# Kernel tuning notes

Hardware: AMD Instinct MI355X
Metric: run time of the kernel (lower is better)

The kernel has to match this reference:

```python
import jax, jax.numpy as jnp
import numpy as np

THETA = 10000.0
EPS = 1e-6

def _rope_tables(n, d):
    # 2D image RoPE: square grid side x side, half of head-dim rotates with
    # row position, half with column position. rotate-half pairing (i, i+d/2).
    side = int(np.sqrt(n))
    dq = d // 4  # angle count per spatial axis
    inv_freq = 1.0 / (THETA ** (np.arange(dq, dtype=np.float32) / dq))
    ang = np.arange(side, dtype=np.float32)[:, None] * inv_freq[None, :]  # [side, dq]
    row = np.broadcast_to(ang[:, None, :], (side, side, dq)).reshape(n, dq)
    col = np.broadcast_to(ang[None, :, :], (side, side, dq)).reshape(n, dq)
    angles = np.concatenate([row, col], axis=-1)  # [n, d//2]
    return jnp.asarray(np.cos(angles)), jnp.asarray(np.sin(angles))

def _apply_rope(t, cos, sin):
    # t: [b, h, n, d]; cos/sin: [n, d//2]
    d2 = t.shape[-1] // 2
    t1, t2 = t[..., :d2], t[..., d2:]
    return jnp.concatenate([t1 * cos - t2 * sin, t1 * sin + t2 * cos], axis=-1)

def _rmsnorm(t, scale):
    var = jnp.mean(t * t, axis=-1, keepdims=True)
    return t * jax.lax.rsqrt(var + EPS) * scale

def setup_inputs() -> dict:
    key = jax.random.key(0)
    ks = jax.random.split(key, 3)
    B, N, D = 8, 1024, 1024
    x = jax.random.normal(ks[0], (B, N, D), dtype=jnp.float32)
    Wqkv = jax.random.normal(ks[1], (D, 3 * D), dtype=jnp.float32) * (D ** -0.5)
    bqkv = jnp.zeros((3 * D,), dtype=jnp.float32)
    Wout = jax.random.normal(ks[2], (D, D), dtype=jnp.float32) * (D ** -0.5)
    bout = jnp.zeros((D,), dtype=jnp.float32)
    hd = D // 16
    return {"x": x, "Wqkv": Wqkv, "bqkv": bqkv, "Wout": Wout, "bout": bout,
            "q_scale": jnp.ones((hd,), jnp.float32), "k_scale": jnp.ones((hd,), jnp.float32)}

def reference(x, Wqkv, bqkv, Wout, bout, q_scale, k_scale):
    B, N, D = x.shape
    H = 16
    hd = D // H
    qkv = x @ Wqkv + bqkv  # [B, N, 3D]
    qkv = qkv.reshape(B, N, 3, H, hd).transpose(2, 0, 3, 1, 4)  # [3, B, H, N, hd]
    q, k, v = qkv[0], qkv[1], qkv[2]
    q = _rmsnorm(q, q_scale)
    k = _rmsnorm(k, k_scale)
    cos, sin = _rope_tables(N, hd)
    q = _apply_rope(q, cos, sin)
    k = _apply_rope(k, cos, sin)
    scale = hd ** -0.5
    scores = jnp.einsum('bhqd,bhkd->bhqk', q, k) * scale
    attn = jax.nn.softmax(scores, axis=-1)
    o = jnp.einsum('bhqk,bhkd->bhqd', attn, v)  # [B, H, N, hd]
    o = o.transpose(0, 2, 1, 3).reshape(B, N, D)
    return o @ Wout + bout
```

## Files before the change

kernel.cpp:

```cpp
#include <hip/hip_runtime.h>
#include <hip/hip_bf16.h>
#include <hip/hip_fp16.h>
#include <math.h>

#define QSZ 8388608

typedef short bf16x8 __attribute__((ext_vector_type(8)));
typedef _Float16 f16x8 __attribute__((ext_vector_type(8)));
typedef float f32x4 __attribute__((ext_vector_type(4)));

__device__ __forceinline__ unsigned short f2bf(float f) {
  __hip_bfloat16 h = __float2bfloat16(f);
  return *reinterpret_cast<unsigned short*>(&h);
}

__device__ __forceinline__ void gload16(const void* g, void* l) {
  __builtin_amdgcn_global_load_lds(
      (const __attribute__((address_space(1))) void*)g,
      (__attribute__((address_space(3))) void*)l, 16, 0, 0);
}

__global__ __launch_bounds__(256)
void cvt_all(const float* __restrict__ x, unsigned short* __restrict__ xb,
             const float* __restrict__ Wq, unsigned short* __restrict__ wqT,
             const float* __restrict__ Wo, unsigned short* __restrict__ woT) {
  __shared__ unsigned short tile[32][33];
  const int bid = blockIdx.x;
  const int t = threadIdx.x;
  if (bid < 4096) {
    const int i = (bid * 256 + t) * 8;
    const float4 a = *(const float4*)&x[i];
    const float4 b = *(const float4*)&x[i + 4];
    ushort4 lo, hi;
    lo.x = f2bf(a.x); lo.y = f2bf(a.y); lo.z = f2bf(a.z); lo.w = f2bf(a.w);
    hi.x = f2bf(b.x); hi.y = f2bf(b.y); hi.z = f2bf(b.z); hi.w = f2bf(b.w);
    *(ushort4*)&xb[i] = lo;
    *(ushort4*)&xb[i + 4] = hi;
    return;
  }
  const float* src;
  unsigned short* dst;
  int bx, by, N;
  if (bid < 7168) {
    src = Wq; dst = wqT; N = 3072;
    bx = (bid - 4096) % 96; by = (bid - 4096) / 96;
  } else {
    src = Wo; dst = woT; N = 1024;
    bx = (bid - 7168) % 32; by = (bid - 7168) / 32;
  }
  const int k0 = by * 32, n0 = bx * 32;
  const int r = t >> 3, c4 = (t & 7) * 4;
  const float4 v = *(const float4*)&src[(k0 + r) * N + n0 + c4];
  tile[r][c4 + 0] = f2bf(v.x);
  tile[r][c4 + 1] = f2bf(v.y);
  tile[r][c4 + 2] = f2bf(v.z);
  tile[r][c4 + 3] = f2bf(v.w);
  __syncthreads();
  ushort4 o;
  o.x = tile[c4 + 0][r];
  o.y = tile[c4 + 1][r];
  o.z = tile[c4 + 2][r];
  o.w = tile[c4 + 3][r];
  *(ushort4*)&dst[(long)(n0 + r) * 1024 + k0 + c4] = o;
}

template<int MODE>
__global__ __launch_bounds__(512, 2)
void gemm256(const unsigned short* __restrict__ A,
             const unsigned short* __restrict__ Bt,
             const float* __restrict__ bias,
             float* __restrict__ Cf,
             __half* __restrict__ Ch,
             const float* __restrict__ qsc,
             const float* __restrict__ ksc) {
  __shared__ __align__(16) unsigned short As[2][16384];
  __shared__ __align__(16) unsigned short Bs[2][16384];
  __shared__ float2 Tab[512];

  constexpr int GXN = (MODE == 0) ? 12 : 4;
  constexpr int CPX = (MODE == 0) ? 48 : 16;

  const int t = threadIdx.x;
  const int swz = (blockIdx.x & 7) * CPX + (blockIdx.x >> 3);
  const int bm = swz / GXN, bn = swz % GXN;
  const int w = t >> 6, lane = t & 63;
  const int M0 = (w >> 2) * 128, N0 = (w & 3) * 64;
  const int lm = lane & 15, q4 = lane >> 4;

  if (MODE == 0) {
    const int pos = t >> 4, idx = t & 15;
    const float invf = expf(-(float)idx * 0.57564627324851149f);
    const float ang = (float)pos * invf;
    Tab[t] = make_float2(cosf(ang), sinf(ang));
  }

  const int c8 = ((t & 7) ^ ((t >> 3) & 7)) << 3;
  const unsigned short* aSrc = A + (long)(bm * 256 + (t >> 3)) * 1024 + c8;
  const unsigned short* bSrc = Bt + (long)(bn * 256 + (t >> 3)) * 1024 + c8;
  unsigned short* lA[2] = {&As[0][t * 8], &As[1][t * 8]};
  unsigned short* lB[2] = {&Bs[0][t * 8], &Bs[1][t * 8]};

  f32x4 acc[8][4] = {};

  auto stage = [&](int buf, int kt) {
    const unsigned short* a = aSrc + kt * 64;
    const unsigned short* b = bSrc + kt * 64;
    unsigned short* la = lA[buf];
    unsigned short* lb = lB[buf];
#pragma unroll
    for (int j = 0; j < 4; ++j) {
      gload16(a + j * 65536, la + j * 4096);
      gload16(b + j * 65536, lb + j * 4096);
    }
  };

  auto compute = [&](const unsigned short* Ac, const unsigned short* Bc) {
#pragma unroll
    for (int kk = 0; kk < 2; ++kk) {
      bf16x8 af[8], bg[4];
#pragma unroll
      for (int mi = 0; mi < 8; ++mi) {
        const int row = M0 + mi * 16 + lm;
        af[mi] = *(const bf16x8*)
            &Ac[row * 64 + ((((kk << 2) + q4) ^ (row & 7)) << 3)];
      }
#pragma unroll
      for (int ni = 0; ni < 4; ++ni) {
        const int row = N0 + ni * 16 + lm;
        bg[ni] = *(const bf16x8*)
            &Bc[row * 64 + ((((kk << 2) + q4) ^ (row & 7)) << 3)];
      }
#pragma unroll
      for (int mi = 0; mi < 8; ++mi)
#pragma unroll
        for (int ni = 0; ni < 4; ++ni)
          acc[mi][ni] = __builtin_amdgcn_mfma_f32_16x16x32_bf16(
              af[mi], bg[ni], acc[mi][ni], 0, 0, 0);
    }
  };

  stage(0, 0);
  stage(1, 1);
  asm volatile("s_waitcnt vmcnt(8)" ::: "memory");
  __builtin_amdgcn_s_barrier();

  for (int kt = 0; kt < 14; ++kt) {
    const int s = kt & 1;
    compute(s ? &As[1][0] : &As[0][0], s ? &Bs[1][0] : &Bs[0][0]);
    asm volatile("s_waitcnt lgkmcnt(0)" ::: "memory");
    __builtin_amdgcn_s_barrier();
    stage(s, kt + 2);
    asm volatile("s_waitcnt vmcnt(8)" ::: "memory");
    __builtin_amdgcn_s_barrier();
  }
  compute(&As[0][0], &Bs[0][0]);
  asm volatile("s_waitcnt lgkmcnt(0)" ::: "memory");
  __builtin_amdgcn_s_barrier();
  asm volatile("s_waitcnt vmcnt(0)" ::: "memory");
  __builtin_amdgcn_s_barrier();
  compute(&As[1][0], &Bs[1][0]);

  const int r0 = q4 << 2;
  const int nb = bn * 256 + N0;

  if (MODE == 1) {
#pragma unroll
    for (int mi = 0; mi < 8; ++mi)
#pragma unroll
      for (int ni = 0; ni < 4; ++ni) {
        const int n = nb + ni * 16 + lm;
        const float bvv = bias[n];
#pragma unroll
        for (int r = 0; r < 4; ++r)
          Cf[(long)(bm * 256 + M0 + mi * 16 + r0 + r) * 1024 + n] =
              acc[mi][ni][r] + bvv;
      }
    return;
  }

  const int tq = nb >> 10, h = (nb >> 6) & 15;

  if (tq == 2) {
#pragma unroll
    for (int mi = 0; mi < 8; ++mi)
#pragma unroll
      for (int ni = 0; ni < 4; ++ni) {
        const int col = nb + ni * 16 + lm;
        const int dd = col & 63;
        const float bv = bias[col];
#pragma unroll
        for (int r = 0; r < 4; ++r) {
          const int m = bm * 256 + M0 + mi * 16 + r0 + r;
          const int b = m >> 10, nn = m & 1023;
          Ch[2L * QSZ + ((long)((b * 16 + h) * 64 + dd)) * 1024 + nn] =
              __float2half(acc[mi][ni][r] + bv);
        }
      }
    return;
  }

  const float* scp = (tq == 0) ? qsc : ksc;
  const float qmul = (tq == 0) ? 0.18033688011112042f : 1.0f;
  float scv[4], bv[4];
#pragma unroll
  for (int ni = 0; ni < 4; ++ni) {
    scv[ni] = scp[ni * 16 + lm];
    bv[ni] = bias[nb + ni * 16 + lm];
  }
  __half* base = Ch + (long)tq * QSZ;
#pragma unroll
  for (int mi = 0; mi < 8; ++mi) {
#pragma unroll
    for (int r = 0; r < 4; ++r) {
      const float v0 = acc[mi][0][r] + bv[0];
      const float v1 = acc[mi][1][r] + bv[1];
      const float v2 = acc[mi][2][r] + bv[2];
      const float v3 = acc[mi][3][r] + bv[3];
      float ss = v0 * v0 + v1 * v1 + v2 * v2 + v3 * v3;
      ss += __shfl_xor(ss, 1, 64);
      ss += __shfl_xor(ss, 2, 64);
      ss += __shfl_xor(ss, 4, 64);
      ss += __shfl_xor(ss, 8, 64);
      const float inv = rsqrtf(ss * (1.0f / 64.0f) + 1e-6f) * qmul;
      const float a0 = v0 * inv * scv[0];
      const float a1 = v1 * inv * scv[1];
      const float a2 = v2 * inv * scv[2];
      const float a3 = v3 * inv * scv[3];
      const int m = bm * 256 + M0 + mi * 16 + r0 + r;
      const int b = m >> 10, nn = m & 1023;
      const float2 tr = Tab[(nn >> 5) * 16 + lm];
      const float2 tc = Tab[(nn & 31) * 16 + lm];
      __half* row = base + ((long)((b * 16 + h) * 1024 + nn)) * 64 + lm;
      row[0]  = __float2half(a0 * tr.x - a2 * tr.y);
      row[16] = __float2half(a1 * tc.x - a3 * tc.y);
      row[32] = __float2half(a0 * tr.y + a2 * tr.x);
      row[48] = __float2half(a1 * tc.y + a3 * tc.x);
    }
  }
}

__global__ __launch_bounds__(256, 3)
void attn_mfma(const __half* __restrict__ qh, const __half* __restrict__ kh,
               const __half* __restrict__ vh, unsigned short* __restrict__ ob) {
  __shared__ __align__(16) __half Ks[2][4096];
  __shared__ __align__(16) __half Vs[2][4096];
  __shared__ __align__(16) __half Pl[8][1152];
  const int t = threadIdx.x;
  const int w = t >> 6, lane = t & 63;
  const int flat = blockIdx.x + blockIdx.y * 8;
  const int xcd = flat & 7, j = flat >> 3;
  const int bh = xcd * 16 + (j >> 3);
  const int qt = j & 7;
  const int lm = lane & 15, q4 = lane >> 4;

  f16x8 qf[2][2];
#pragma unroll
  for (int g = 0; g < 2; ++g) {
    const __half* qrow =
        qh + ((long)(bh * 1024 + qt * 128 + g * 64 + w * 16 + lm)) * 64 +
        q4 * 8;
    qf[g][0] = *(const f16x8*)qrow;
    qf[g][1] = *(const f16x8*)(qrow + 32);
  }

  f32x4 o[2][4] = {};
  float l_r[2][4] = {};

  const int prow = t >> 3, pc = t & 7;
  const int scz = pc ^ (prow & 7);
  const __half* ksrc0 = kh + (long)(bh * 1024 + prow) * 64 + scz * 8;
  const __half* vsrc0 = vh + (long)(bh * 64 + prow) * 1024 + scz * 8;

  gload16(ksrc0, &Ks[0][t * 8]);
  gload16(ksrc0 + 32 * 64, &Ks[0][2048 + t * 8]);
  gload16(vsrc0, &Vs[0][t * 8]);
  gload16(vsrc0 + 32 * 1024, &Vs[0][2048 + t * 8]);

  for (int kc = 0; kc < 16; ++kc) {
    const int cur = kc & 1;
    __syncthreads();

    if (kc < 15) {
      const int nx = cur ^ 1;
      const __half* ksrc = ksrc0 + (kc + 1) * 4096;
      const __half* vsrc = vsrc0 + (kc + 1) * 64;
      gload16(ksrc, &Ks[nx][t * 8]);
      gload16(ksrc + 32 * 64, &Ks[nx][2048 + t * 8]);
      gload16(vsrc, &Vs[nx][t * 8]);
      gload16(vsrc + 32 * 1024, &Vs[nx][2048 + t * 8]);
    }

    f16x8 kf[4][2];
#pragma unroll
    for (int nt = 0; nt < 4; ++nt) {
      const int kr = nt * 16 + lm;
#pragma unroll
      for (int ks = 0; ks < 2; ++ks)
        kf[nt][ks] = *(const f16x8*)&Ks[cur][kr * 64 +
                                      (((ks << 2) + q4) ^ (kr & 7)) * 8];
    }

#pragma unroll
    for (int g = 0; g < 2; ++g) {
      f32x4 s[4];
      __builtin_amdgcn_s_setprio(1);
#pragma unroll
      for (int nt = 0; nt < 4; ++nt) {
        s[nt] = (f32x4){0.f, 0.f, 0.f, 0.f};
#pragma unroll
        for (int ks = 0; ks < 2; ++ks)
          s[nt] = __builtin_amdgcn_mfma_f32_16x16x32_f16(qf[g][ks], kf[nt][ks],
                                                         s[nt], 0, 0, 0);
      }
      __builtin_amdgcn_s_setprio(0);
      __half* Pw = &Pl[w * 2 + g][0];
#pragma unroll
      for (int nt = 0; nt < 4; ++nt) {
#pragma unroll
        for (int r = 0; r < 4; ++r) {
          const float p = exp2f(s[nt][r] - 12.98425536800067f);
          l_r[g][r] += p;
          Pw[(q4 * 4 + r) * 72 + nt * 16 + lm] = (__half)p;
        }
      }
    }

    __builtin_amdgcn_s_setprio(1);
#pragma unroll
    for (int ks2 = 0; ks2 < 2; ++ks2) {
      const f16x8 pf0 = *(const f16x8*)&Pl[w * 2 + 0][lm * 72 + ks2 * 32 +
                                                      q4 * 8];
      const f16x8 pf1 = *(const f16x8*)&Pl[w * 2 + 1][lm * 72 + ks2 * 32 +
                                                      q4 * 8];
#pragma unroll
      for (int nt = 0; nt < 4; ++nt) {
        const int dr = nt * 16 + lm;
        const f16x8 vf = *(const f16x8*)&Vs[cur][dr * 64 +
                                          (((ks2 << 2) + q4) ^ (dr & 7)) * 8];
        o[0][nt] = __builtin_amdgcn_mfma_f32_16x16x32_f16(pf0, vf, o[0][nt],
                                                          0, 0, 0);
        o[1][nt] = __builtin_amdgcn_mfma_f32_16x16x32_f16(pf1, vf, o[1][nt],
                                                          0, 0, 0);
      }
    }
    __builtin_amdgcn_s_setprio(0);
  }

  const int b = bh >> 4, h = bh & 15;
#pragma unroll
  for (int g = 0; g < 2; ++g) {
#pragma unroll
    for (int r = 0; r < 4; ++r) {
      float l = l_r[g][r];
      l += __shfl_xor(l, 1, 64);
      l += __shfl_xor(l, 2, 64);
      l += __shfl_xor(l, 4, 64);
      l += __shfl_xor(l, 8, 64);
      const float linv = 1.0f / l;
      const long rowg =
          (long)(b * 1024 + qt * 128 + g * 64 + w * 16 + q4 * 4 + r) * 1024 +
          h * 64;
#pragma unroll
      for (int nt = 0; nt < 4; ++nt)
        ob[rowg + nt * 16 + lm] = f2bf(o[g][nt][r] * linv);
    }
  }
}

extern "C" void kernel_launch(void* const* d_in, const int* in_sizes, int n_in,
                              void* d_out, int out_size, void* d_ws,
                              size_t ws_size, hipStream_t stream) {
  const float* x    = (const float*)d_in[0];
  const float* Wqkv = (const float*)d_in[1];
  const float* bqkv = (const float*)d_in[2];
  const float* Wout = (const float*)d_in[3];
  const float* bout = (const float*)d_in[4];
  const float* qs   = (const float*)d_in[5];
  const float* ks   = (const float*)d_in[6];
  float* out = (float*)d_out;
  float* W = (float*)d_ws;

  __half* qkvh = (__half*)W;
  __half* qpre = qkvh;
  __half* kpre = qkvh + QSZ;
  __half* vT   = qkvh + 2 * QSZ;
  unsigned short* xb  = (unsigned short*)(W + 12582912);
  unsigned short* ob  = xb;
  unsigned short* wqT = (unsigned short*)(W + 16777216);
  unsigned short* woT = wqT + 3 * 1024 * 1024;

  cvt_all<<<8192, 256, 0, stream>>>(x, xb, Wqkv, wqT, Wout, woT);
  gemm256<0><<<384, 512, 0, stream>>>(xb, wqT, bqkv, nullptr, qkvh, qs, ks);
  attn_mfma<<<dim3(8, 128), 256, 0, stream>>>(qpre, kpre, vT, ob);
  gemm256<1><<<128, 512, 0, stream>>>(ob, woT, bout, out, nullptr, nullptr,
                                      nullptr);
}
```

Baseline: 265.1 us.

## Halve output GEMM M-tile for more blocks; transpose QK^T to vectorize P stores

```diff
diff --git a/kernel.cpp b/kernel.cpp
--- a/kernel.cpp
+++ b/kernel.cpp
@@ -7,6 +7,7 @@
 
 typedef short bf16x8 __attribute__((ext_vector_type(8)));
 typedef _Float16 f16x8 __attribute__((ext_vector_type(8)));
+typedef _Float16 f16x4 __attribute__((ext_vector_type(4)));
 typedef float f32x4 __attribute__((ext_vector_type(4)));
 
 __device__ __forceinline__ unsigned short f2bf(float f) {
@@ -73,18 +74,21 @@
              __half* __restrict__ Ch,
              const float* __restrict__ qsc,
              const float* __restrict__ ksc) {
-  __shared__ __align__(16) unsigned short As[2][16384];
+  constexpr int BM  = (MODE == 0) ? 256 : 128;
+  constexpr int AM  = (MODE == 0) ? 8 : 4;
+  constexpr int LA  = BM / 64;
+  constexpr int GXN = (MODE == 0) ? 12 : 4;
+  constexpr int CPX = (MODE == 0) ? 48 : 32;
+
+  __shared__ __align__(16) unsigned short As[2][BM * 64];
   __shared__ __align__(16) unsigned short Bs[2][16384];
   __shared__ float2 Tab[512];
-
-  constexpr int GXN = (MODE == 0) ? 12 : 4;
-  constexpr int CPX = (MODE == 0) ? 48 : 16;
 
   const int t = threadIdx.x;
   const int swz = (blockIdx.x & 7) * CPX + (blockIdx.x >> 3);
   const int bm = swz / GXN, bn = swz % GXN;
   const int w = t >> 6, lane = t & 63;
-  const int M0 = (w >> 2) * 128, N0 = (w & 3) * 64;
+  const int M0 = (w >> 2) * (BM / 2), N0 = (w & 3) * 64;
   const int lm = lane & 15, q4 = lane >> 4;
 
   if (MODE == 0) {
@@ -95,31 +99,34 @@
   }
 
   const int c8 = ((t & 7) ^ ((t >> 3) & 7)) << 3;
-  const unsigned short* aSrc = A + (long)(bm * 256 + (t >> 3)) * 1024 + c8;
+  const unsigned short* aSrc = A + (long)(bm * BM + (t >> 3)) * 1024 + c8;
   const unsigned short* bSrc = Bt + (long)(bn * 256 + (t >> 3)) * 1024 + c8;
-  unsigned short* lA[2] = {&As[0][t * 8], &As[1][t * 8]};
-  unsigned short* lB[2] = {&Bs[0][t * 8], &Bs[1][t * 8]};
-
-  f32x4 acc[8][4] = {};
+
+  f32x4 acc[AM][4] = {};
 
   auto stage = [&](int buf, int kt) {
     const unsigned short* a = aSrc + kt * 64;
     const unsigned short* b = bSrc + kt * 64;
-    unsigned short* la = lA[buf];
-    unsigned short* lb = lB[buf];
-#pragma unroll
-    for (int j = 0; j < 4; ++j) {
-      gload16(a + j * 65536, la + j * 4096);
-      gload16(b + j * 65536, lb + j * 4096);
-    }
+#pragma unroll
+    for (int j = 0; j < LA; ++j)
+      gload16(a + j * 65536, &As[buf][t * 8 + j * 4096]);
+#pragma unroll
+    for (int j = 0; j < 4; ++j)
+      gload16(b + j * 65536, &Bs[buf][t * 8 + j * 4096]);
   };
+  auto waitTile = [] {
+    if constexpr (MODE == 0)
+      asm volatile("s_waitcnt vmcnt(8)" ::: "memory");
+    else
+      asm volatile("s_waitcnt vmcnt(6)" ::: "memory");
+  };
 
   auto compute = [&](const unsigned short* Ac, const unsigned short* Bc) {
 #pragma unroll
     for (int kk = 0; kk < 2; ++kk) {
-      bf16x8 af[8], bg[4];
-#pragma unroll
-      for (int mi = 0; mi < 8; ++mi) {
+      bf16x8 af[AM], bg[4];
+#pragma unroll
+      for (int mi = 0; mi < AM; ++mi) {
         const int row = M0 + mi * 16 + lm;
         af[mi] = *(const bf16x8*)
             &Ac[row * 64 + ((((kk << 2) + q4) ^ (row & 7)) << 3)];
@@ -131,7 +138,7 @@
             &Bc[row * 64 + ((((kk << 2) + q4) ^ (row & 7)) << 3)];
       }
 #pragma unroll
-      for (int mi = 0; mi < 8; ++mi)
+      for (int mi = 0; mi < AM; ++mi)
 #pragma unroll
         for (int ni = 0; ni < 4; ++ni)
           acc[mi][ni] = __builtin_amdgcn_mfma_f32_16x16x32_bf16(
@@ -141,7 +148,7 @@
 
   stage(0, 0);
   stage(1, 1);
-  asm volatile("s_waitcnt vmcnt(8)" ::: "memory");
+  waitTile();
   __builtin_amdgcn_s_barrier();
 
   for (int kt = 0; kt < 14; ++kt) {
@@ -150,7 +157,7 @@
     asm volatile("s_waitcnt lgkmcnt(0)" ::: "memory");
     __builtin_amdgcn_s_barrier();
     stage(s, kt + 2);
-    asm volatile("s_waitcnt vmcnt(8)" ::: "memory");
+    waitTile();
     __builtin_amdgcn_s_barrier();
   }
   compute(&As[0][0], &Bs[0][0]);
@@ -165,14 +172,14 @@
 
   if (MODE == 1) {
 #pragma unroll
-    for (int mi = 0; mi < 8; ++mi)
+    for (int mi = 0; mi < AM; ++mi)
 #pragma unroll
       for (int ni = 0; ni < 4; ++ni) {
         const int n = nb + ni * 16 + lm;
         const float bvv = bias[n];
 #pragma unroll
         for (int r = 0; r < 4; ++r)
-          Cf[(long)(bm * 256 + M0 + mi * 16 + r0 + r) * 1024 + n] =
+          Cf[(long)(bm * BM + M0 + mi * 16 + r0 + r) * 1024 + n] =
               acc[mi][ni][r] + bvv;
       }
     return;
@@ -182,7 +189,7 @@
 
   if (tq == 2) {
 #pragma unroll
-    for (int mi = 0; mi < 8; ++mi)
+    for (int mi = 0; mi < AM; ++mi)
 #pragma unroll
       for (int ni = 0; ni < 4; ++ni) {
         const int col = nb + ni * 16 + lm;
@@ -190,7 +197,7 @@
         const float bv = bias[col];
 #pragma unroll
         for (int r = 0; r < 4; ++r) {
-          const int m = bm * 256 + M0 + mi * 16 + r0 + r;
+          const int m = bm * BM + M0 + mi * 16 + r0 + r;
           const int b = m >> 10, nn = m & 1023;
           Ch[2L * QSZ + ((long)((b * 16 + h) * 64 + dd)) * 1024 + nn] =
               __float2half(acc[mi][ni][r] + bv);
@@ -209,7 +216,7 @@
   }
   __half* base = Ch + (long)tq * QSZ;
 #pragma unroll
-  for (int mi = 0; mi < 8; ++mi) {
+  for (int mi = 0; mi < AM; ++mi) {
 #pragma unroll
     for (int r = 0; r < 4; ++r) {
       const float v0 = acc[mi][0][r] + bv[0];
@@ -226,7 +233,7 @@
       const float a1 = v1 * inv * scv[1];
       const float a2 = v2 * inv * scv[2];
       const float a3 = v3 * inv * scv[3];
-      const int m = bm * 256 + M0 + mi * 16 + r0 + r;
+      const int m = bm * BM + M0 + mi * 16 + r0 + r;
       const int b = m >> 10, nn = m & 1023;
       const float2 tr = Tab[(nn >> 5) * 16 + lm];
       const float2 tc = Tab[(nn & 31) * 16 + lm];
@@ -264,7 +271,7 @@
   }
 
   f32x4 o[2][4] = {};
-  float l_r[2][4] = {};
+  float l_r[2] = {};
 
   const int prow = t >> 3, pc = t & 7;
   const int scz = pc ^ (prow & 7);
@@ -309,20 +316,25 @@
         s[nt] = (f32x4){0.f, 0.f, 0.f, 0.f};
 #pragma unroll
         for (int ks = 0; ks < 2; ++ks)
-          s[nt] = __builtin_amdgcn_mfma_f32_16x16x32_f16(qf[g][ks], kf[nt][ks],
+          s[nt] = __builtin_amdgcn_mfma_f32_16x16x32_f16(kf[nt][ks], qf[g][ks],
                                                          s[nt], 0, 0, 0);
       }
       __builtin_amdgcn_s_setprio(0);
       __half* Pw = &Pl[w * 2 + g][0];
+      float lacc = 0.f;
 #pragma unroll
       for (int nt = 0; nt < 4; ++nt) {
-#pragma unroll
-        for (int r = 0; r < 4; ++r) {
-          const float p = exp2f(s[nt][r] - 12.98425536800067f);
-          l_r[g][r] += p;
-          Pw[(q4 * 4 + r) * 72 + nt * 16 + lm] = (__half)p;
-        }
-      }
+        const float p0 = exp2f(s[nt][0] - 12.98425536800067f);
+        const float p1 = exp2f(s[nt][1] - 12.98425536800067f);
+        const float p2 = exp2f(s[nt][2] - 12.98425536800067f);
+        const float p3 = exp2f(s[nt][3] - 12.98425536800067f);
+        lacc += (p0 + p1) + (p2 + p3);
+        f16x4 pv;
+        pv[0] = (_Float16)p0; pv[1] = (_Float16)p1;
+        pv[2] = (_Float16)p2; pv[3] = (_Float16)p3;
+        *(f16x4*)&Pw[lm * 72 + nt * 16 + q4 * 4] = pv;
+      }
+      l_r[g] += lacc;
     }
 
     __builtin_amdgcn_s_setprio(1);
@@ -349,14 +361,13 @@
   const int b = bh >> 4, h = bh & 15;
 #pragma unroll
   for (int g = 0; g < 2; ++g) {
+    float l = l_r[g];
+    l += __shfl_xor(l, 16, 64);
+    l += __shfl_xor(l, 32, 64);
+    const float linv_row = 1.0f / l;
 #pragma unroll
     for (int r = 0; r < 4; ++r) {
-      float l = l_r[g][r];
-      l += __shfl_xor(l, 1, 64);
-      l += __shfl_xor(l, 2, 64);
-      l += __shfl_xor(l, 4, 64);
-      l += __shfl_xor(l, 8, 64);
-      const float linv = 1.0f / l;
+      const float linv = __shfl(linv_row, q4 * 4 + r, 64);
       const long rowg =
           (long)(b * 1024 + qt * 128 + g * 64 + w * 16 + q4 * 4 + r) * 1024 +
           h * 64;
@@ -392,6 +403,6 @@
   cvt_all<<<8192, 256, 0, stream>>>(x, xb, Wqkv, wqT, Wout, woT);
   gemm256<0><<<384, 512, 0, stream>>>(xb, wqT, bqkv, nullptr, qkvh, qs, ks);
   attn_mfma<<<dim3(8, 128), 256, 0, stream>>>(qpre, kpre, vT, ob);
-  gemm256<1><<<128, 512, 0, stream>>>(ob, woT, bout, out, nullptr, nullptr,
+  gemm256<1><<<256, 512, 0, stream>>>(ob, woT, bout, out, nullptr, nullptr,
                                       nullptr);
 }
```

Result: faster. 252.9 us (-4.6%).
